# Kernel tuning notes

Hardware: AMD Instinct MI355X
Metric: run time of the kernel (lower is better)

## Reference

```python
import jax, jax.numpy as jnp
import numpy as np
from jax import lax

V, T, E, H, K = 100000, 4096, 256, 512, 32
Hh = H // 2  # per-direction LSTM hidden


def setup_inputs() -> dict:
    ks = jax.random.split(jax.random.key(0), 16)
    def rn(i, shape, scale=0.1):
        return jax.random.normal(ks[i], shape, dtype=jnp.float32) * scale
    return {
        "sent": jax.random.randint(ks[0], (T,), 0, V),
        "embed": rn(1, (V, E)),
        "Wih_f": rn(2, (4 * Hh, E)), "Whh_f": rn(3, (4 * Hh, Hh)),
        "bih_f": rn(4, (4 * Hh,)), "bhh_f": rn(5, (4 * Hh,)),
        "Wih_b": rn(6, (4 * Hh, E)), "Whh_b": rn(7, (4 * Hh, Hh)),
        "bih_b": rn(8, (4 * Hh,)), "bhh_b": rn(9, (4 * Hh,)),
        "h0": rn(10, (2, Hh)), "c0": rn(11, (2, Hh)),
        "W_out": rn(12, (K, H)), "b_out": rn(13, (K,)),
        "transitions": rn(14, (K, K)),
    }


def _lstm_dir(x, h0, c0, Wih, Whh, bih, bhh):
    # x: (T, E) -> hs: (T, Hh). PyTorch LSTM gate order: i, f, g, o.
    def step(carry, xt):
        h, c = carry
        g = xt @ Wih.T + h @ Whh.T + bih + bhh  # (4*Hh,)
        i, f, gg, o = jnp.split(g, 4)
        c = jax.nn.sigmoid(f) * c + jax.nn.sigmoid(i) * jnp.tanh(gg)
        h = jax.nn.sigmoid(o) * jnp.tanh(c)
        return (h, c), h
    _, hs = lax.scan(step, (h0, c0), x)
    return hs


def _feats(sent, embed, Wih_f, Whh_f, bih_f, bhh_f, Wih_b, Whh_b, bih_b, bhh_b, h0, c0, W_out, b_out):
    x = embed[sent]                                              # (T, E)
    hf = _lstm_dir(x, h0[0], c0[0], Wih_f, Whh_f, bih_f, bhh_f)  # (T, Hh)
    hb = _lstm_dir(x[::-1], h0[1], c0[1], Wih_b, Whh_b, bih_b, bhh_b)[::-1]
    h = jnp.concatenate([hf, hb], axis=-1)                       # (T, H)
    return h @ W_out.T + b_out                                   # (T, K)


def _viterbi(feats, trans):
    # scores[i, j] = prev[i] + trans[i, j] + obs[j]; max/argmax over previous tag i.
    def step(prev, obs):
        scores = prev[:, None] + trans + obs[None, :]  # (K, K)
        best = jnp.max(scores, axis=0)
        ix = jnp.argmax(scores, axis=0)
        return best, (best, ix)
    last, (alphas, ixs) = lax.scan(step, feats[0], feats[1:])
    cur = jnp.argmax(last)
    score = jnp.max(last)
    def back(c, ix_row):
        pre = ix_row[c]
        return pre, pre
    _, prevs = lax.scan(back, cur, ixs, reverse=True)
    path = jnp.concatenate([prevs, cur[None]])  # (T,)
    return path, score


def reference(sent, embed, Wih_f, Whh_f, bih_f, bhh_f, Wih_b, Whh_b, bih_b, bhh_b, h0, c0, W_out, b_out, transitions):
    feats = _feats(sent, embed, Wih_f, Whh_f, bih_f, bhh_f,
                   Wih_b, Whh_b, bih_b, bhh_b, h0, c0, W_out, b_out)
    path, score = _viterbi(feats, transitions)
    return path, score
```

## Files before the change

kernel.cpp:

```cpp
#include <hip/hip_runtime.h>
#include <stdint.h>

#define T_LEN 4096
#define E_DIM 256
#define HH 256

typedef unsigned long long u64;

__device__ __forceinline__ float sigmoidf_(float x) {
    return __builtin_amdgcn_rcpf(1.0f + __expf(-x));
}
__device__ __forceinline__ float tanh_fast(float x) {
    float e = __expf(2.0f * x);
    return 1.0f - 2.0f * __builtin_amdgcn_rcpf(e + 1.0f);
}

template <int CTRL>
__device__ __forceinline__ float dpp_add(float x) {
    int t = __builtin_amdgcn_update_dpp(0, __float_as_int(x), CTRL, 0xF, 0xF, true);
    return x + __int_as_float(t);
}

__global__ __launch_bounds__(256) void proj_kernel(
    const int* __restrict__ sent, const float* __restrict__ embed,
    const float* __restrict__ Wih_f, const float* __restrict__ bih_f, const float* __restrict__ bhh_f,
    const float* __restrict__ Wih_b, const float* __restrict__ bih_b, const float* __restrict__ bhh_b,
    float* __restrict__ gates_f, float* __restrict__ gates_b)
{
    __shared__ float4 xt[16][64];
    const int tid = threadIdx.x;
    const int dir = blockIdx.y;
    const int t0  = blockIdx.x * 16;

    const float* Wih = dir ? Wih_b : Wih_f;
    const float* bih = dir ? bih_b : bih_f;
    const float* bhh = dir ? bhh_b : bhh_f;
    float* gates     = dir ? gates_b : gates_f;

    {
        int row = tid >> 4;
        int c   = tid & 15;
        const float4* src = (const float4*)(embed + (size_t)sent[t0 + row] * E_DIM);
        xt[row][c]      = src[c];
        xt[row][c + 16] = src[c + 16];
        xt[row][c + 32] = src[c + 32];
        xt[row][c + 48] = src[c + 48];
    }
    __syncthreads();

    float acc[4][16];
    #pragma unroll
    for (int ri = 0; ri < 4; ++ri)
        #pragma unroll
        for (int tt = 0; tt < 16; ++tt) acc[ri][tt] = 0.f;

    const float4* wrow0 = (const float4*)(Wih + (size_t)(0 * 256 + tid) * 256);
    const float4* wrow1 = (const float4*)(Wih + (size_t)(1 * 256 + tid) * 256);
    const float4* wrow2 = (const float4*)(Wih + (size_t)(2 * 256 + tid) * 256);
    const float4* wrow3 = (const float4*)(Wih + (size_t)(3 * 256 + tid) * 256);

    for (int k4 = 0; k4 < 64; ++k4) {
        float4 xv[16];
        #pragma unroll
        for (int tt = 0; tt < 16; ++tt) xv[tt] = xt[tt][k4];
        float4 w0 = wrow0[k4], w1 = wrow1[k4], w2 = wrow2[k4], w3 = wrow3[k4];
        #pragma unroll
        for (int tt = 0; tt < 16; ++tt) {
            acc[0][tt] += w0.x*xv[tt].x + w0.y*xv[tt].y + w0.z*xv[tt].z + w0.w*xv[tt].w;
            acc[1][tt] += w1.x*xv[tt].x + w1.y*xv[tt].y + w1.z*xv[tt].z + w1.w*xv[tt].w;
            acc[2][tt] += w2.x*xv[tt].x + w2.y*xv[tt].y + w2.z*xv[tt].z + w2.w*xv[tt].w;
            acc[3][tt] += w3.x*xv[tt].x + w3.y*xv[tt].y + w3.z*xv[tt].z + w3.w*xv[tt].w;
        }
    }

    #pragma unroll
    for (int ri = 0; ri < 4; ++ri) {
        int r = ri * 256 + tid;
        float b = bih[r] + bhh[r];
        #pragma unroll
        for (int tt = 0; tt < 16; ++tt)
            gates[(size_t)(t0 + tt) * 1024 + r] = acc[ri][tt] + b;
    }
}

__global__ __launch_bounds__(512, 1) void lstm_kernel(
    const float* __restrict__ Whh_f, const float* __restrict__ Whh_b,
    const float* __restrict__ gates_f, const float* __restrict__ gates_b,
    const float* __restrict__ h0, const float* __restrict__ c0,
    float* __restrict__ h_out, u64* __restrict__ msg)
{
    const int xcd  = blockIdx.x & 7;
    const int slot = blockIdx.x >> 3;
    if (xcd > 1) return;
    const int dir = xcd;
    const int g   = slot;

    const int tid = threadIdx.x;
    const int jl  = tid >> 4;
    const int s   = tid & 15;
    const int j   = g * 32 + jl;
    const int f   = (s + (s >> 3)) & 7;

    const float* Whh   = dir ? Whh_b : Whh_f;
    const float* gates = dir ? gates_b : gates_f;

    float w[64];
    #pragma unroll
    for (int gg = 0; gg < 4; ++gg) {
        const float2* row2 = (const float2*)(Whh + (size_t)(gg * 256 + j) * 256 + s * 16);
        #pragma unroll
        for (int i = 0; i < 8; ++i) {
            float2 v = row2[(3 * i + f) & 7];
            w[gg * 16 + i * 2 + 0] = v.x;
            w[gg * 16 + i * 2 + 1] = v.y;
        }
    }
    #pragma unroll
    for (int k = 0; k < 64; ++k)
        asm volatile("" : "+a"(w[k]));

    int off[8];
    #pragma unroll
    for (int i = 0; i < 8; ++i)
        off[i] = s * 64 + ((3 * i + f) & 7) * 8;

    __shared__ __align__(16) float h_lds[2][256];

    float c = 0.f;
    if (tid < 32) {
        int j0 = g * 32 + tid;
        float h = h0[dir * HH + j0];
        h_lds[0][j0] = h;
        u64 p = ((u64)1u << 32) | (u64)__float_as_uint(h);
        __hip_atomic_store(&msg[(0 * 2 + dir) * 256 + j0], p,
                           __ATOMIC_RELAXED, __HIP_MEMORY_SCOPE_AGENT);
    }
    if (s == 0) c = c0[dir * HH + j];

    float gin0 = 0.f, gin1 = 0.f, gin2 = 0.f, gin3 = 0.f;
    if (s == 0) {
        const int tf0 = dir ? (T_LEN - 1) : 0;
        const float* gp = gates + (size_t)tf0 * 1024 + j;
        gin0 = gp[0]; gin1 = gp[256]; gin2 = gp[512]; gin3 = gp[768];
    }

    for (int t = 0; t < T_LEN; ++t) {
        const int tf = dir ? (T_LEN - 1 - t) : t;

        float ng0 = 0.f, ng1 = 0.f, ng2 = 0.f, ng3 = 0.f;
        if (s == 0 && t + 1 < T_LEN) {
            const int tfn = dir ? (T_LEN - 2 - t) : (t + 1);
            const float* gp = gates + (size_t)tfn * 1024 + j;
            ng0 = gp[0]; ng1 = gp[256]; ng2 = gp[512]; ng3 = gp[768];
        }

        if (tid < 256 && (tid >> 5) != g) {
            u64* sp = &msg[((t & 1) * 2 + dir) * 256 + tid];
            const unsigned want = (unsigned)(t + 1);
            u64 m;
            do {
                m = __hip_atomic_load(sp, __ATOMIC_RELAXED, __HIP_MEMORY_SCOPE_AGENT);
            } while ((unsigned)(m >> 32) != want);
            h_lds[t & 1][tid] = __uint_as_float((unsigned)m);
        }
        __syncthreads();

        const char* hb = (const char*)(&h_lds[t & 1][0]);
        float p0 = 0.f, p1 = 0.f, p2 = 0.f, p3 = 0.f;
        #pragma unroll
        for (int i = 0; i < 8; ++i) {
            float2 h2 = *(const float2*)(hb + off[i]);
            p0 += w[i*2+0]*h2.x + w[i*2+1]*h2.y;
            p1 += w[16+i*2+0]*h2.x + w[16+i*2+1]*h2.y;
            p2 += w[32+i*2+0]*h2.x + w[32+i*2+1]*h2.y;
            p3 += w[48+i*2+0]*h2.x + w[48+i*2+1]*h2.y;
        }

        p0 = dpp_add<0xB1>(p0);  p1 = dpp_add<0xB1>(p1);
        p2 = dpp_add<0xB1>(p2);  p3 = dpp_add<0xB1>(p3);
        p0 = dpp_add<0x4E>(p0);  p1 = dpp_add<0x4E>(p1);
        p2 = dpp_add<0x4E>(p2);  p3 = dpp_add<0x4E>(p3);
        p0 = dpp_add<0x141>(p0); p1 = dpp_add<0x141>(p1);
        p2 = dpp_add<0x141>(p2); p3 = dpp_add<0x141>(p3);
        p0 = dpp_add<0x140>(p0); p1 = dpp_add<0x140>(p1);
        p2 = dpp_add<0x140>(p2); p3 = dpp_add<0x140>(p3);

        if (s == 0) {
            float iv = sigmoidf_(gin0 + p0);
            float fv = sigmoidf_(gin1 + p1);
            float gv = tanh_fast(gin2 + p2);
            float ov = sigmoidf_(gin3 + p3);
            c = fv * c + iv * gv;
            float h = ov * tanh_fast(c);
            u64 pck = ((u64)(unsigned)(t + 2) << 32) | (u64)__float_as_uint(h);
            __hip_atomic_store(&msg[(((t + 1) & 1) * 2 + dir) * 256 + j], pck,
                               __ATOMIC_RELAXED, __HIP_MEMORY_SCOPE_AGENT);
            h_lds[(t + 1) & 1][j] = h;
            h_out[(size_t)tf * 512 + dir * HH + j] = h;
        }
        gin0 = ng0; gin1 = ng1; gin2 = ng2; gin3 = ng3;
    }
}

__global__ __launch_bounds__(64) void feats_kernel(
    const float* __restrict__ h_out, const float* __restrict__ W_out,
    const float* __restrict__ b_out, float* __restrict__ feats)
{
    const int t = blockIdx.x;
    const int lane = threadIdx.x;
    const int k = lane >> 1, half = lane & 1;
    const float4* hv = (const float4*)(h_out + (size_t)t * 512 + half * 256);
    const float4* wv = (const float4*)(W_out + (size_t)k * 512 + half * 256);
    float p = 0.f;
    #pragma unroll 16
    for (int i = 0; i < 64; ++i) {
        float4 a = hv[i], b = wv[i];
        p += a.x*b.x + a.y*b.y + a.z*b.z + a.w*b.w;
    }
    p += __shfl_xor(p, 1);
    if (half == 0) feats[t * 32 + k] = p + b_out[k];
}

#define VT_CHUNK 128
__global__ __launch_bounds__(64) void viterbi_kernel(
    const float* __restrict__ feats, const float* __restrict__ trans,
    float* __restrict__ out)
{
    extern __shared__ unsigned char dynls[];
    unsigned char* ixs = dynls;
    float* fchunk = (float*)(dynls + 131072);
    __shared__ float fin[32];

    const int lane = threadIdx.x;
    const int j = lane >> 1, ih = lane & 1;

    float ttr[16];
    #pragma unroll
    for (int q = 0; q < 16; ++q) ttr[q] = trans[(ih * 16 + q) * 32 + j];

    float alpha = 0.f;

    for (int cs = 0; cs < T_LEN; cs += VT_CHUNK) {
        const float4* src = (const float4*)(feats + (size_t)cs * 32);
        float4* dst = (float4*)fchunk;
        #pragma unroll
        for (int i = 0; i < 16; ++i) dst[lane + 64 * i] = src[lane + 64 * i];
        __syncthreads();

        int tbeg = cs;
        if (cs == 0) { alpha = fchunk[j]; tbeg = 1; }

        for (int t = tbeg; t < cs + VT_CHUNK; ++t) {
            float obs = fchunk[(t - cs) * 32 + j];
            float v[16]; int ix[16];
            #pragma unroll
            for (int q = 0; q < 16; ++q) {
                int i = ih * 16 + q;
                v[q] = (__shfl(alpha, 2 * i) + ttr[q]) + obs;
                ix[q] = i;
            }
            #pragma unroll
            for (int st = 8; st >= 1; st >>= 1)
                #pragma unroll
                for (int q = 0; q < 8; ++q)
                    if (q < st && v[q + st] > v[q]) { v[q] = v[q + st]; ix[q] = ix[q + st]; }
            float best = v[0]; int barg = ix[0];

            float ob = __shfl_xor(best, 1); int oa = __shfl_xor(barg, 1);
            float m0 = ih ? ob : best; int a0 = ih ? oa : barg;
            float m1 = ih ? best : ob; int a1 = ih ? barg : oa;
            float m = m0; int a = a0;
            if (m1 > m0) { m = m1; a = a1; }
            if (ih == 0) ixs[(t - 1) * 32 + j] = (unsigned char)a;
            alpha = m;
        }
        __syncthreads();
    }

    if (ih == 0) fin[j] = alpha;
    __syncthreads();

    if (lane == 0) {
        float sc = fin[0]; int cur = 0;
        for (int q = 1; q < 32; ++q)
            if (fin[q] > sc) { sc = fin[q]; cur = q; }
        out[T_LEN] = sc;
        out[T_LEN - 1] = (float)cur;
        for (int t = T_LEN - 2; t >= 0; --t) {
            cur = ixs[t * 32 + cur];
            out[t] = (float)cur;
        }
    }
}

extern "C" void kernel_launch(void* const* d_in, const int* in_sizes, int n_in,
                              void* d_out, int out_size, void* d_ws, size_t ws_size,
                              hipStream_t stream) {
    const int*   sent  = (const int*)d_in[0];
    const float* embed = (const float*)d_in[1];
    const float* Wih_f = (const float*)d_in[2];
    const float* Whh_f = (const float*)d_in[3];
    const float* bih_f = (const float*)d_in[4];
    const float* bhh_f = (const float*)d_in[5];
    const float* Wih_b = (const float*)d_in[6];
    const float* Whh_b = (const float*)d_in[7];
    const float* bih_b = (const float*)d_in[8];
    const float* bhh_b = (const float*)d_in[9];
    const float* h0    = (const float*)d_in[10];
    const float* c0    = (const float*)d_in[11];
    const float* W_out = (const float*)d_in[12];
    const float* b_out = (const float*)d_in[13];
    const float* trans = (const float*)d_in[14];
    float* out = (float*)d_out;

    float* gates_f = (float*)d_ws;
    float* gates_b = gates_f + (size_t)T_LEN * 1024;
    float* h_out   = gates_b + (size_t)T_LEN * 1024;
    float* feats   = h_out   + (size_t)T_LEN * 512;
    u64*   msg     = (u64*)(feats + (size_t)T_LEN * 32);

    dim3 gproj(T_LEN / 16, 2);
    proj_kernel<<<gproj, 256, 0, stream>>>(sent, embed,
        Wih_f, bih_f, bhh_f, Wih_b, bih_b, bhh_b, gates_f, gates_b);

    lstm_kernel<<<64, 512, 0, stream>>>(Whh_f, Whh_b, gates_f, gates_b,
                                        h0, c0, h_out, msg);

    feats_kernel<<<T_LEN, 64, 0, stream>>>(h_out, W_out, b_out, feats);

    hipFuncSetAttribute((const void*)viterbi_kernel,
                        hipFuncAttributeMaxDynamicSharedMemorySize, 147456);
    viterbi_kernel<<<1, 64, 147456, stream>>>(feats, trans, out);
}
```

Measured before the change: 6.496 ms.

## Poll neighbour hidden state with vector loads and drop LDS staging in LSTM

Each thread now polls its 16-element slice of the previous hidden state straight from a second global message buffer, using eight vector loads with the sc0 cache modifier, and checks all step tags at once. This removes the LDS staging and the single-element atomic polling per lane. The gate nonlinearity is computed redundantly by all lanes, and the next-step gate prefetch becomes unconditional. An atomic fallback path takes over after many spins. The Viterbi kernel now shares alpha through LDS instead of shuffles and adds the observation once after the max, which may change tie-breaking slightly.

```diff
diff --git a/kernel.cpp b/kernel.cpp
--- a/kernel.cpp
+++ b/kernel.cpp
@@ -6,6 +6,7 @@
 #define HH 256
 
 typedef unsigned long long u64;
+typedef float f32x4 __attribute__((ext_vector_type(4)));
 
 __device__ __forceinline__ float sigmoidf_(float x) {
     return __builtin_amdgcn_rcpf(1.0f + __expf(-x));
@@ -87,7 +88,7 @@
     const float* __restrict__ Whh_f, const float* __restrict__ Whh_b,
     const float* __restrict__ gates_f, const float* __restrict__ gates_b,
     const float* __restrict__ h0, const float* __restrict__ c0,
-    float* __restrict__ h_out, u64* __restrict__ msg)
+    float* __restrict__ h_out, u64* __restrict__ msg, u64* __restrict__ msgf)
 {
     const int xcd  = blockIdx.x & 7;
     const int slot = blockIdx.x >> 3;
@@ -99,7 +100,6 @@
     const int jl  = tid >> 4;
     const int s   = tid & 15;
     const int j   = g * 32 + jl;
-    const int f   = (s + (s >> 3)) & 7;
 
     const float* Whh   = dir ? Whh_b : Whh_f;
     const float* gates = dir ? gates_b : gates_f;
@@ -107,73 +107,115 @@
     float w[64];
     #pragma unroll
     for (int gg = 0; gg < 4; ++gg) {
-        const float2* row2 = (const float2*)(Whh + (size_t)(gg * 256 + j) * 256 + s * 16);
-        #pragma unroll
-        for (int i = 0; i < 8; ++i) {
-            float2 v = row2[(3 * i + f) & 7];
-            w[gg * 16 + i * 2 + 0] = v.x;
-            w[gg * 16 + i * 2 + 1] = v.y;
+        const float4* row = (const float4*)(Whh + (size_t)(gg * 256 + j) * 256 + s * 16);
+        #pragma unroll
+        for (int i = 0; i < 4; ++i) {
+            float4 v = row[i];
+            w[gg * 16 + i * 4 + 0] = v.x;
+            w[gg * 16 + i * 4 + 1] = v.y;
+            w[gg * 16 + i * 4 + 2] = v.z;
+            w[gg * 16 + i * 4 + 3] = v.w;
         }
     }
     #pragma unroll
     for (int k = 0; k < 64; ++k)
         asm volatile("" : "+a"(w[k]));
 
-    int off[8];
-    #pragma unroll
-    for (int i = 0; i < 8; ++i)
-        off[i] = s * 64 + ((3 * i + f) & 7) * 8;
-
-    __shared__ __align__(16) float h_lds[2][256];
-
-    float c = 0.f;
-    if (tid < 32) {
-        int j0 = g * 32 + tid;
-        float h = h0[dir * HH + j0];
-        h_lds[0][j0] = h;
-        u64 p = ((u64)1u << 32) | (u64)__float_as_uint(h);
-        __hip_atomic_store(&msg[(0 * 2 + dir) * 256 + j0], p,
+    float c = c0[dir * HH + j];
+
+    if (s == 0) {
+        float hinit = h0[dir * HH + j];
+        u64 p1 = ((u64)1u << 32) | (u64)__float_as_uint(hinit);
+        u64* z1f = msgf + (size_t)(1 * 2 + dir) * 256 + j;
+        asm volatile("global_store_dwordx2 %0, %1, off sc0"
+                     :: "v"((u64)(uintptr_t)z1f), "v"(0ull) : "memory");
+        __hip_atomic_store(&msg[(1 * 2 + dir) * 256 + j], 0ull,
                            __ATOMIC_RELAXED, __HIP_MEMORY_SCOPE_AGENT);
-    }
-    if (s == 0) c = c0[dir * HH + j];
-
-    float gin0 = 0.f, gin1 = 0.f, gin2 = 0.f, gin3 = 0.f;
-    if (s == 0) {
-        const int tf0 = dir ? (T_LEN - 1) : 0;
-        const float* gp = gates + (size_t)tf0 * 1024 + j;
-        gin0 = gp[0]; gin1 = gp[256]; gin2 = gp[512]; gin3 = gp[768];
-    }
+        __threadfence();
+        u64* f0 = msgf + (size_t)(0 * 2 + dir) * 256 + j;
+        asm volatile("global_store_dwordx2 %0, %1, off sc0"
+                     :: "v"((u64)(uintptr_t)f0), "v"(p1) : "memory");
+        __hip_atomic_store(&msg[(0 * 2 + dir) * 256 + j], p1,
+                           __ATOMIC_RELAXED, __HIP_MEMORY_SCOPE_AGENT);
+    }
+
+    const ptrdiff_t dstep = dir ? -1024 : 1024;
+    const float* gp = gates + (size_t)(dir ? (T_LEN - 1) : 0) * 1024 + j;
+    float gin0 = gp[0], gin1 = gp[256], gin2 = gp[512], gin3 = gp[768];
+
+    const u64 pb0 = (u64)(uintptr_t)(msgf + (size_t)(0 * 2 + dir) * 256 + s * 16);
+    const u64 pb1 = (u64)(uintptr_t)(msgf + (size_t)(1 * 2 + dir) * 256 + s * 16);
+    const u64* sb0 = msg + (size_t)(0 * 2 + dir) * 256 + s * 16;
+    const u64* sb1 = msg + (size_t)(1 * 2 + dir) * 256 + s * 16;
+
+    int fastmode = 1;
 
     for (int t = 0; t < T_LEN; ++t) {
         const int tf = dir ? (T_LEN - 1 - t) : t;
-
-        float ng0 = 0.f, ng1 = 0.f, ng2 = 0.f, ng3 = 0.f;
-        if (s == 0 && t + 1 < T_LEN) {
-            const int tfn = dir ? (T_LEN - 2 - t) : (t + 1);
-            const float* gp = gates + (size_t)tfn * 1024 + j;
-            ng0 = gp[0]; ng1 = gp[256]; ng2 = gp[512]; ng3 = gp[768];
-        }
-
-        if (tid < 256 && (tid >> 5) != g) {
-            u64* sp = &msg[((t & 1) * 2 + dir) * 256 + tid];
-            const unsigned want = (unsigned)(t + 1);
-            u64 m;
-            do {
-                m = __hip_atomic_load(sp, __ATOMIC_RELAXED, __HIP_MEMORY_SCOPE_AGENT);
-            } while ((unsigned)(m >> 32) != want);
-            h_lds[t & 1][tid] = __uint_as_float((unsigned)m);
+        const unsigned want = (unsigned)(t + 1);
+
+        float hv[16];
+        if (fastmode) {
+            const u64 pb = (t & 1) ? pb1 : pb0;
+            int spins = 0;
+            for (;;) {
+                f32x4 q0, q1, q2, q3, q4, q5, q6, q7;
+                asm volatile(
+                    "global_load_dwordx4 %0, %8, off sc0\n\t"
+                    "global_load_dwordx4 %1, %8, off offset:16 sc0\n\t"
+                    "global_load_dwordx4 %2, %8, off offset:32 sc0\n\t"
+                    "global_load_dwordx4 %3, %8, off offset:48 sc0\n\t"
+                    "global_load_dwordx4 %4, %8, off offset:64 sc0\n\t"
+                    "global_load_dwordx4 %5, %8, off offset:80 sc0\n\t"
+                    "global_load_dwordx4 %6, %8, off offset:96 sc0\n\t"
+                    "global_load_dwordx4 %7, %8, off offset:112 sc0\n\t"
+                    "s_waitcnt vmcnt(0)"
+                    : "=&v"(q0), "=&v"(q1), "=&v"(q2), "=&v"(q3),
+                      "=&v"(q4), "=&v"(q5), "=&v"(q6), "=&v"(q7)
+                    : "v"(pb)
+                    : "memory");
+                unsigned d;
+                d  = (__float_as_uint(q0.y) ^ want) | (__float_as_uint(q0.w) ^ want);
+                d |= (__float_as_uint(q1.y) ^ want) | (__float_as_uint(q1.w) ^ want);
+                d |= (__float_as_uint(q2.y) ^ want) | (__float_as_uint(q2.w) ^ want);
+                d |= (__float_as_uint(q3.y) ^ want) | (__float_as_uint(q3.w) ^ want);
+                d |= (__float_as_uint(q4.y) ^ want) | (__float_as_uint(q4.w) ^ want);
+                d |= (__float_as_uint(q5.y) ^ want) | (__float_as_uint(q5.w) ^ want);
+                d |= (__float_as_uint(q6.y) ^ want) | (__float_as_uint(q6.w) ^ want);
+                d |= (__float_as_uint(q7.y) ^ want) | (__float_as_uint(q7.w) ^ want);
+                if (d == 0) {
+                    hv[0]  = q0.x; hv[1]  = q0.z; hv[2]  = q1.x; hv[3]  = q1.z;
+                    hv[4]  = q2.x; hv[5]  = q2.z; hv[6]  = q3.x; hv[7]  = q3.z;
+                    hv[8]  = q4.x; hv[9]  = q4.z; hv[10] = q5.x; hv[11] = q5.z;
+                    hv[12] = q6.x; hv[13] = q6.z; hv[14] = q7.x; hv[15] = q7.z;
+                    break;
+                }
+                if (++spins > 1024) { fastmode = 0; break; }
+            }
+        }
+        if (!fastmode) {
+            const u64* sb = (t & 1) ? sb1 : sb0;
+            #pragma unroll
+            for (int i = 0; i < 16; ++i) {
+                u64 m;
+                do {
+                    m = __hip_atomic_load(&sb[i], __ATOMIC_RELAXED, __HIP_MEMORY_SCOPE_AGENT);
+                } while ((unsigned)(m >> 32) != want);
+                hv[i] = __uint_as_float((unsigned)m);
+            }
         }
         __syncthreads();
 
-        const char* hb = (const char*)(&h_lds[t & 1][0]);
+        const float* gn = gp + dstep;
+        float ng0 = gn[0], ng1 = gn[256], ng2 = gn[512], ng3 = gn[768];
+
         float p0 = 0.f, p1 = 0.f, p2 = 0.f, p3 = 0.f;
         #pragma unroll
-        for (int i = 0; i < 8; ++i) {
-            float2 h2 = *(const float2*)(hb + off[i]);
-            p0 += w[i*2+0]*h2.x + w[i*2+1]*h2.y;
-            p1 += w[16+i*2+0]*h2.x + w[16+i*2+1]*h2.y;
-            p2 += w[32+i*2+0]*h2.x + w[32+i*2+1]*h2.y;
-            p3 += w[48+i*2+0]*h2.x + w[48+i*2+1]*h2.y;
+        for (int cix = 0; cix < 16; ++cix) {
+            p0 += w[cix]      * hv[cix];
+            p1 += w[16 + cix] * hv[cix];
+            p2 += w[32 + cix] * hv[cix];
+            p3 += w[48 + cix] * hv[cix];
         }
 
         p0 = dpp_add<0xB1>(p0);  p1 = dpp_add<0xB1>(p1);
@@ -185,20 +227,25 @@
         p0 = dpp_add<0x140>(p0); p1 = dpp_add<0x140>(p1);
         p2 = dpp_add<0x140>(p2); p3 = dpp_add<0x140>(p3);
 
+        float iv = sigmoidf_(gin0 + p0);
+        float fv = sigmoidf_(gin1 + p1);
+        float gv = tanh_fast(gin2 + p2);
+        float ov = sigmoidf_(gin3 + p3);
+        c = fv * c + iv * gv;
+        float h = ov * tanh_fast(c);
+
         if (s == 0) {
-            float iv = sigmoidf_(gin0 + p0);
-            float fv = sigmoidf_(gin1 + p1);
-            float gv = tanh_fast(gin2 + p2);
-            float ov = sigmoidf_(gin3 + p3);
-            c = fv * c + iv * gv;
-            float h = ov * tanh_fast(c);
             u64 pck = ((u64)(unsigned)(t + 2) << 32) | (u64)__float_as_uint(h);
+            u64* fp = msgf + (size_t)(((t + 1) & 1) * 2 + dir) * 256 + j;
+            asm volatile("global_store_dwordx2 %0, %1, off sc0"
+                         :: "v"((u64)(uintptr_t)fp), "v"(pck) : "memory");
             __hip_atomic_store(&msg[(((t + 1) & 1) * 2 + dir) * 256 + j], pck,
                                __ATOMIC_RELAXED, __HIP_MEMORY_SCOPE_AGENT);
-            h_lds[(t + 1) & 1][j] = h;
-            h_out[(size_t)tf * 512 + dir * HH + j] = h;
-        }
+        }
+        if (s == 1) h_out[(size_t)tf * 512 + dir * HH + j] = h;
+
         gin0 = ng0; gin1 = ng1; gin2 = ng2; gin3 = ng3;
+        gp = gn;
     }
 }
 
@@ -229,6 +276,7 @@
     extern __shared__ unsigned char dynls[];
     unsigned char* ixs = dynls;
     float* fchunk = (float*)(dynls + 131072);
+    __shared__ __align__(16) float alf[32];
     __shared__ float fin[32];
 
     const int lane = threadIdx.x;
@@ -251,14 +299,25 @@
         if (cs == 0) { alpha = fchunk[j]; tbeg = 1; }
 
         for (int t = tbeg; t < cs + VT_CHUNK; ++t) {
+            if (ih == 0) alf[j] = alpha;
             float obs = fchunk[(t - cs) * 32 + j];
+            float4 a0 = *(const float4*)&alf[ih * 16 + 0];
+            float4 a1 = *(const float4*)&alf[ih * 16 + 4];
+            float4 a2 = *(const float4*)&alf[ih * 16 + 8];
+            float4 a3 = *(const float4*)&alf[ih * 16 + 12];
+
             float v[16]; int ix[16];
+            v[0]  = a0.x + ttr[0];  v[1]  = a0.y + ttr[1];
+            v[2]  = a0.z + ttr[2];  v[3]  = a0.w + ttr[3];
+            v[4]  = a1.x + ttr[4];  v[5]  = a1.y + ttr[5];
+            v[6]  = a1.z + ttr[6];  v[7]  = a1.w + ttr[7];
+            v[8]  = a2.x + ttr[8];  v[9]  = a2.y + ttr[9];
+            v[10] = a2.z + ttr[10]; v[11] = a2.w + ttr[11];
+            v[12] = a3.x + ttr[12]; v[13] = a3.y + ttr[13];
+            v[14] = a3.z + ttr[14]; v[15] = a3.w + ttr[15];
             #pragma unroll
-            for (int q = 0; q < 16; ++q) {
-                int i = ih * 16 + q;
-                v[q] = (__shfl(alpha, 2 * i) + ttr[q]) + obs;
-                ix[q] = i;
-            }
+            for (int q = 0; q < 16; ++q) ix[q] = ih * 16 + q;
+
             #pragma unroll
             for (int st = 8; st >= 1; st >>= 1)
                 #pragma unroll
@@ -267,12 +326,12 @@
             float best = v[0]; int barg = ix[0];
 
             float ob = __shfl_xor(best, 1); int oa = __shfl_xor(barg, 1);
-            float m0 = ih ? ob : best; int a0 = ih ? oa : barg;
-            float m1 = ih ? best : ob; int a1 = ih ? barg : oa;
-            float m = m0; int a = a0;
-            if (m1 > m0) { m = m1; a = a1; }
+            float m0 = ih ? ob : best; int a0i = ih ? oa : barg;
+            float m1 = ih ? best : ob; int a1i = ih ? barg : oa;
+            float m = m0; int a = a0i;
+            if (m1 > m0) { m = m1; a = a1i; }
             if (ih == 0) ixs[(t - 1) * 32 + j] = (unsigned char)a;
-            alpha = m;
+            alpha = m + obs;
         }
         __syncthreads();
     }
@@ -318,13 +377,14 @@
     float* h_out   = gates_b + (size_t)T_LEN * 1024;
     float* feats   = h_out   + (size_t)T_LEN * 512;
     u64*   msg     = (u64*)(feats + (size_t)T_LEN * 32);
+    u64*   msgf    = msg + 1024;
 
     dim3 gproj(T_LEN / 16, 2);
     proj_kernel<<<gproj, 256, 0, stream>>>(sent, embed,
         Wih_f, bih_f, bhh_f, Wih_b, bih_b, bhh_b, gates_f, gates_b);
 
     lstm_kernel<<<64, 512, 0, stream>>>(Whh_f, Whh_b, gates_f, gates_b,
-                                        h0, c0, h_out, msg);
+                                        h0, c0, h_out, msg, msgf);
 
     feats_kernel<<<T_LEN, 64, 0, stream>>>(h_out, W_out, b_out, feats);
 
```

After: 24.97 ms. 3.84x slower.
